# Performance work log

Hardware: AMD Instinct MI355X
Metric: run time of the kernel (lower is better)

## Reference

```python
import jax, jax.numpy as jnp
import numpy as np

B, T, D = 4, 2048, 1024
H, DH = 16, 64

def setup_inputs() -> dict:
    key = jax.random.key(0)
    k1, k2, k3 = jax.random.split(key, 3)
    x = jax.random.normal(k1, (B, T, D), dtype=jnp.float32)
    # nn.Linear weights stored [out, in]; we keep that convention
    w_attn = jax.random.normal(k2, (3 * D, D), dtype=jnp.float32) * (1.0 / np.sqrt(D))
    w_proj = jax.random.normal(k3, (D, D), dtype=jnp.float32) * (1.0 / np.sqrt(D))
    return {"x": x, "w_attn": w_attn, "w_proj": w_proj}

def reference(x, w_attn, w_proj):
    Bx, Tx, Dx = x.shape
    qkv = jnp.einsum('btd,ed->bte', x, w_attn)            # [B,T,3D]
    qkv = qkv.reshape(Bx, Tx, 3, H, DH)
    q = qkv[:, :, 0].transpose(0, 2, 1, 3)                # [B,H,T,DH]
    k = qkv[:, :, 1].transpose(0, 2, 1, 3)
    v = qkv[:, :, 2].transpose(0, 2, 1, 3)
    scale = 1.0 / np.sqrt(DH).astype(np.float32)
    att = jnp.einsum('bhqd,bhkd->bhqk', q, k) * scale     # [B,H,T,T]
    causal = jnp.tril(jnp.ones((Tx, Tx), dtype=bool))
    att = jnp.where(causal[None, None], att, jnp.float32(-jnp.inf))
    att = jax.nn.softmax(att, axis=-1)
    y = jnp.einsum('bhqk,bhkd->bhqd', att, v)             # [B,H,T,DH]
    y = y.transpose(0, 2, 1, 3).reshape(Bx, Tx, Dx)       # [B,T,D]
    y = jnp.einsum('btd,ed->bte', y, w_proj)
    return y
```

## Files before the change

kernel.cpp:

```cpp
#include <hip/hip_runtime.h>

typedef unsigned short u16;
typedef __bf16 bf16x8 __attribute__((ext_vector_type(8)));
typedef float floatx4 __attribute__((ext_vector_type(4)));

__device__ inline u16 f2bf(float x) {
    unsigned int u = __builtin_bit_cast(unsigned int, x);
    return (u16)((u + 0x7FFFu + ((u >> 16) & 1u)) >> 16);
}

__device__ inline floatx4 fzero() {
    floatx4 z = {0.f, 0.f, 0.f, 0.f};
    return z;
}

#if defined(__has_builtin)
#if __has_builtin(__builtin_amdgcn_exp2f)
#define EXP2F(x) __builtin_amdgcn_exp2f(x)
#endif
#endif
#ifndef EXP2F
#define EXP2F(x) exp2f(x)
#endif

template <bool F32>
__device__ inline bf16x8 ld8(const void* base, size_t off) {
    if constexpr (F32) {
        const float* p = (const float*)base + off;
        float4 a = *(const float4*)p;
        float4 b = *(const float4*)(p + 4);
        union { u16 u[8]; bf16x8 v; } t;
        t.u[0] = f2bf(a.x); t.u[1] = f2bf(a.y); t.u[2] = f2bf(a.z); t.u[3] = f2bf(a.w);
        t.u[4] = f2bf(b.x); t.u[5] = f2bf(b.y); t.u[6] = f2bf(b.z); t.u[7] = f2bf(b.w);
        return t.v;
    } else {
        return *(const bf16x8*)((const u16*)base + off);
    }
}

__global__ __launch_bounds__(256) void cvt_f32_bf16(const float* __restrict__ src,
                                                    u16* __restrict__ dst, int n8) {
    int i = blockIdx.x * 256 + threadIdx.x;
    if (i >= n8) return;
    dst += (size_t)i * 8;
    *(bf16x8*)dst = ld8<true>(src, (size_t)i * 8);
}

#define BK 32

template <bool AF32, bool BF32, bool CF32>
__global__ __launch_bounds__(256) void gemm_bt(const void* __restrict__ Ap,
                                               const void* __restrict__ Bp,
                                               void* __restrict__ Cp,
                                               int M, int N, int K) {
    __shared__ alignas(16) u16 As[128 * BK];
    __shared__ alignas(16) u16 Bs[128 * BK];

    const int tid  = threadIdx.x;
    const int lane = tid & 63;
    const int wave = tid >> 6;
    const int wm = (wave >> 1) * 64;
    const int wn = (wave & 1) * 64;
    const int tm = blockIdx.y * 128;
    const int tn = blockIdx.x * 128;
    const int l15 = lane & 15;
    const int l4  = lane >> 4;

    const int srow = tid >> 2;
    const int scol = (tid & 3) * 8;

    floatx4 acc[4][4];
#pragma unroll
    for (int i = 0; i < 4; i++)
#pragma unroll
        for (int j = 0; j < 4; j++) acc[i][j] = fzero();

    for (int k0 = 0; k0 < K; k0 += BK) {
        bf16x8 av[2], bv[2];
#pragma unroll
        for (int q = 0; q < 2; q++) {
            av[q] = ld8<AF32>(Ap, (size_t)(tm + srow + q * 64) * K + k0 + scol);
            bv[q] = ld8<BF32>(Bp, (size_t)(tn + srow + q * 64) * K + k0 + scol);
        }
        __syncthreads();
#pragma unroll
        for (int q = 0; q < 2; q++) {
            *(bf16x8*)&As[(srow + q * 64) * BK + scol] = av[q];
            *(bf16x8*)&Bs[(srow + q * 64) * BK + scol] = bv[q];
        }
        __syncthreads();

        bf16x8 af[4], bf[4];
#pragma unroll
        for (int i = 0; i < 4; i++)
            af[i] = *(const bf16x8*)&As[(wm + i * 16 + l15) * BK + l4 * 8];
#pragma unroll
        for (int j = 0; j < 4; j++)
            bf[j] = *(const bf16x8*)&Bs[(wn + j * 16 + l15) * BK + l4 * 8];
#pragma unroll
        for (int i = 0; i < 4; i++)
#pragma unroll
            for (int j = 0; j < 4; j++)
                acc[i][j] = __builtin_amdgcn_mfma_f32_16x16x32_bf16(af[i], bf[j], acc[i][j], 0, 0, 0);
    }

#pragma unroll
    for (int i = 0; i < 4; i++)
#pragma unroll
        for (int j = 0; j < 4; j++)
#pragma unroll
            for (int r = 0; r < 4; r++) {
                int row = tm + wm + i * 16 + l4 * 4 + r;
                int col = tn + wn + j * 16 + l15;
                if constexpr (CF32)
                    ((float*)Cp)[(size_t)row * N + col] = acc[i][j][r];
                else
                    ((u16*)Cp)[(size_t)row * N + col] = f2bf(acc[i][j][r]);
            }
}

__global__ __launch_bounds__(256) void transpose_v(const u16* __restrict__ qkv,
                                                   u16* __restrict__ vT) {
    __shared__ alignas(16) u16 Ts[64 * 80];
    const int bh = blockIdx.x;
    const int b = bh >> 4, h = bh & 15;
    const int t0 = blockIdx.y * 64;
    const int tid = threadIdx.x;
    const int r = tid >> 3;
    const int c = tid & 7;
#pragma unroll
    for (int p = 0; p < 2; p++) {
        int tr = r + p * 32;
        *(bf16x8*)&Ts[tr * 80 + c * 8] =
            *(const bf16x8*)&qkv[(size_t)(b * 2048 + t0 + tr) * 3072 + 2048 + h * 64 + c * 8];
    }
    __syncthreads();
#pragma unroll
    for (int p = 0; p < 2; p++) {
        int dr = r + p * 32;
        union { u16 u[8]; bf16x8 v; } t;
#pragma unroll
        for (int i = 0; i < 8; i++) t.u[i] = Ts[(c * 8 + i) * 80 + dr];
        *(bf16x8*)&vT[(size_t)bh * 131072 + (size_t)dr * 2048 + t0 + c * 8] = t.v;
    }
}

#define AST 88

template <bool USE_VT>
__global__ __launch_bounds__(256) void attn2(const u16* __restrict__ qkv,
                                             const u16* __restrict__ vT,
                                             u16* __restrict__ y) {
    const int T = 2048, CW = 3072;
    __shared__ alignas(16) u16 KP[64 * AST];
    __shared__ alignas(16) u16 Vt[64 * AST];

    const int tid  = threadIdx.x;
    const int lane = tid & 63;
    const int wave = tid >> 6;
    const int l15 = lane & 15;
    const int l4  = lane >> 4;

    const int bh = blockIdx.x;
    const int qt = 31 - blockIdx.y;
    const int b = bh >> 4, h = bh & 15;
    const int q0 = qt * 64;

    const size_t base = (size_t)b * T * CW + h * 64;
    const u16* qp = qkv + base;
    const u16* kp = qkv + base + 1024;
    const u16* vp = qkv + base + 2048;
    const u16* vtp = USE_VT ? (vT + (size_t)bh * 131072) : nullptr;

    bf16x8 qf[2];
    {
        int qrow = q0 + wave * 16 + l15;
        qf[0] = *(const bf16x8*)&qp[(size_t)qrow * CW + l4 * 8];
        qf[1] = *(const bf16x8*)&qp[(size_t)qrow * CW + 32 + l4 * 8];
    }

    const float C2 = 0.18033688f;
    float lrow[4] = {0.f, 0.f, 0.f, 0.f};
    floatx4 Oacc[4];
#pragma unroll
    for (int cf = 0; cf < 4; cf++) Oacc[cf] = fzero();

    const int sr = tid >> 3;
    const int sc = tid & 7;

    for (int kt = 0; kt <= qt; kt++) {
        const int t0 = kt * 64;
        __syncthreads();

#pragma unroll
        for (int p = 0; p < 2; p++) {
            int tr = sr + p * 32;
            *(bf16x8*)&KP[tr * AST + sc * 8] =
                *(const bf16x8*)&kp[(size_t)(t0 + tr) * CW + sc * 8];
        }
        if constexpr (USE_VT) {
#pragma unroll
            for (int p = 0; p < 2; p++) {
                int dr = sr + p * 32;
                *(bf16x8*)&Vt[dr * AST + sc * 8] =
                    *(const bf16x8*)&vtp[(size_t)dr * 2048 + t0 + sc * 8];
            }
        } else {
            int dh = tid & 63;
            int tb = (tid >> 6) * 8;
#pragma unroll
            for (int p = 0; p < 2; p++) {
                int tl = tb + p * 32;
                union { u16 u[8]; bf16x8 v; } tmp;
#pragma unroll
                for (int i = 0; i < 8; i++)
                    tmp.u[i] = vp[(size_t)(t0 + tl + i) * CW + dh];
                *(bf16x8*)&Vt[dh * AST + tl] = tmp.v;
            }
        }
        __syncthreads();

        floatx4 sfr[4];
#pragma unroll
        for (int j = 0; j < 4; j++) {
            bf16x8 k0f = *(const bf16x8*)&KP[(j * 16 + l15) * AST + l4 * 8];
            bf16x8 k1f = *(const bf16x8*)&KP[(j * 16 + l15) * AST + 32 + l4 * 8];
            floatx4 s = fzero();
            s = __builtin_amdgcn_mfma_f32_16x16x32_bf16(qf[0], k0f, s, 0, 0, 0);
            s = __builtin_amdgcn_mfma_f32_16x16x32_bf16(qf[1], k1f, s, 0, 0, 0);
            sfr[j] = s;
        }
        bf16x8 v0f[4], v1f[4];
#pragma unroll
        for (int cf = 0; cf < 4; cf++) {
            v0f[cf] = *(const bf16x8*)&Vt[(cf * 16 + l15) * AST + l4 * 8];
            v1f[cf] = *(const bf16x8*)&Vt[(cf * 16 + l15) * AST + 32 + l4 * 8];
        }

        float pj[4][4];
        if (kt == qt) {
#pragma unroll
            for (int j = 0; j < 4; j++)
#pragma unroll
                for (int r = 0; r < 4; r++) {
                    int qrow = q0 + wave * 16 + l4 * 4 + r;
                    int krow = t0 + j * 16 + l15;
                    float e = (krow <= qrow) ? sfr[j][r] * C2 : -1.0e30f;
                    pj[j][r] = EXP2F(e);
                }
        } else {
#pragma unroll
            for (int j = 0; j < 4; j++)
#pragma unroll
                for (int r = 0; r < 4; r++)
                    pj[j][r] = EXP2F(sfr[j][r] * C2);
        }
#pragma unroll
        for (int r = 0; r < 4; r++)
            lrow[r] += (pj[0][r] + pj[1][r]) + (pj[2][r] + pj[3][r]);

        __syncthreads();
#pragma unroll
        for (int j = 0; j < 4; j++)
#pragma unroll
            for (int r = 0; r < 4; r++)
                KP[(wave * 16 + l4 * 4 + r) * AST + j * 16 + l15] = f2bf(pj[j][r]);
        __syncthreads();

        bf16x8 pf0 = *(const bf16x8*)&KP[(wave * 16 + l15) * AST + l4 * 8];
        bf16x8 pf1 = *(const bf16x8*)&KP[(wave * 16 + l15) * AST + 32 + l4 * 8];
#pragma unroll
        for (int cf = 0; cf < 4; cf++) {
            Oacc[cf] = __builtin_amdgcn_mfma_f32_16x16x32_bf16(pf0, v0f[cf], Oacc[cf], 0, 0, 0);
            Oacc[cf] = __builtin_amdgcn_mfma_f32_16x16x32_bf16(pf1, v1f[cf], Oacc[cf], 0, 0, 0);
        }
    }

#pragma unroll
    for (int r = 0; r < 4; r++) {
#pragma unroll
        for (int off = 1; off < 16; off <<= 1)
            lrow[r] += __shfl_xor(lrow[r], off, 64);
    }
#pragma unroll
    for (int r = 0; r < 4; r++) {
        float inv = 1.0f / lrow[r];
        int qrow = q0 + wave * 16 + l4 * 4 + r;
        size_t orow = ((size_t)b * T + qrow) * 1024 + h * 64;
#pragma unroll
        for (int cf = 0; cf < 4; cf++)
            y[orow + cf * 16 + l15] = f2bf(Oacc[cf][r] * inv);
    }
}

extern "C" void kernel_launch(void* const* d_in, const int* in_sizes, int n_in,
                              void* d_out, int out_size, void* d_ws, size_t ws_size,
                              hipStream_t stream) {
    const float* x      = (const float*)d_in[0];
    const float* w_attn = (const float*)d_in[1];
    const float* w_proj = (const float*)d_in[2];
    float* out = (float*)d_out;

    const size_t QKV = (size_t)8192 * 3072;
    const size_t Y   = (size_t)8192 * 1024;
    const size_t VTE = (size_t)64 * 64 * 2048;
    const size_t XB  = (size_t)8192 * 1024;
    const size_t WAB = (size_t)3072 * 1024;
    const size_t WPB = (size_t)1024 * 1024;

    u16* qkv = (u16*)d_ws;
    u16* yb  = qkv + QKV;

    const bool full = ws_size >= (QKV + Y + VTE + XB + WAB + WPB) * sizeof(u16);
    const bool mid  = ws_size >= (QKV + Y + VTE) * sizeof(u16);
    if (ws_size < (QKV + Y) * sizeof(u16)) return;

    dim3 blk(256);
    dim3 g1(3072 / 128, 8192 / 128), g2(1024 / 128, 8192 / 128);
    dim3 ga(64, 32);

    if (full) {
        u16* vT  = yb + Y;
        u16* xb  = vT + VTE;
        u16* wab = xb + XB;
        u16* wpb = wab + WAB;
        cvt_f32_bf16<<<(XB / 8 + 255) / 256, blk, 0, stream>>>(x, xb, (int)(XB / 8));
        cvt_f32_bf16<<<(WAB / 8 + 255) / 256, blk, 0, stream>>>(w_attn, wab, (int)(WAB / 8));
        cvt_f32_bf16<<<(WPB / 8 + 255) / 256, blk, 0, stream>>>(w_proj, wpb, (int)(WPB / 8));
        gemm_bt<false, false, false><<<g1, blk, 0, stream>>>(xb, wab, qkv, 8192, 3072, 1024);
        transpose_v<<<ga, blk, 0, stream>>>(qkv, vT);
        attn2<true><<<ga, blk, 0, stream>>>(qkv, vT, yb);
        gemm_bt<false, false, true><<<g2, blk, 0, stream>>>(yb, wpb, out, 8192, 1024, 1024);
    } else if (mid) {
        u16* vT = yb + Y;
        gemm_bt<true, true, false><<<g1, blk, 0, stream>>>(x, w_attn, qkv, 8192, 3072, 1024);
        transpose_v<<<ga, blk, 0, stream>>>(qkv, vT);
        attn2<true><<<ga, blk, 0, stream>>>(qkv, vT, yb);
        gemm_bt<false, true, true><<<g2, blk, 0, stream>>>(yb, w_proj, out, 8192, 1024, 1024);
    } else {
        gemm_bt<true, true, false><<<g1, blk, 0, stream>>>(x, w_attn, qkv, 8192, 3072, 1024);
        attn2<false><<<ga, blk, 0, stream>>>(qkv, nullptr, yb);
        gemm_bt<false, true, true><<<g2, blk, 0, stream>>>(yb, w_proj, out, 8192, 1024, 1024);
    }
}
```

Baseline: 285.3 us.

## Restructure attention to 128-row query tiles with per-wave P buffers

The attention kernel now handles 128 query rows per block (32 per wave, in two 16-row groups), so each staged K/V tile is reused by twice as many queries. The P tile goes through a per-wave shared buffer, which removes two block-wide barriers per key tile. The kernel computes S transposed (K times Q) and pre-scales Q by the softmax constant, and skips the MFMAs for row groups that lie fully above the causal diagonal. It also writes the output as vectorised bf16x4 stores. In exchange it uses more registers and shared memory (launch bounds 256,4), and the grid has half as many blocks, with more per-block imbalance along the causal diagonal.

```diff
diff --git a/kernel.cpp b/kernel.cpp
--- a/kernel.cpp
+++ b/kernel.cpp
@@ -2,7 +2,9 @@
 
 typedef unsigned short u16;
 typedef __bf16 bf16x8 __attribute__((ext_vector_type(8)));
+typedef __bf16 bf16x4 __attribute__((ext_vector_type(4)));
 typedef float floatx4 __attribute__((ext_vector_type(4)));
+typedef float floatx8 __attribute__((ext_vector_type(8)));
 
 __device__ inline u16 f2bf(float x) {
     unsigned int u = __builtin_bit_cast(unsigned int, x);
@@ -22,6 +24,12 @@
 #ifndef EXP2F
 #define EXP2F(x) exp2f(x)
 #endif
+
+__device__ inline bf16x8 scale8(bf16x8 v, float s) {
+    floatx8 f = __builtin_convertvector(v, floatx8);
+    f *= s;
+    return __builtin_convertvector(f, bf16x8);
+}
 
 template <bool F32>
 __device__ inline bf16x8 ld8(const void* base, size_t off) {
@@ -145,15 +153,17 @@
     }
 }
 
-#define AST 88
+#define AST 72
+#define PST 72
 
 template <bool USE_VT>
-__global__ __launch_bounds__(256) void attn2(const u16* __restrict__ qkv,
-                                             const u16* __restrict__ vT,
-                                             u16* __restrict__ y) {
+__global__ __launch_bounds__(256, 4) void attn3(const u16* __restrict__ qkv,
+                                                const u16* __restrict__ vT,
+                                                u16* __restrict__ y) {
     const int T = 2048, CW = 3072;
-    __shared__ alignas(16) u16 KP[64 * AST];
+    __shared__ alignas(16) u16 Kt[64 * AST];
     __shared__ alignas(16) u16 Vt[64 * AST];
+    __shared__ alignas(16) u16 Pw[4][32 * PST];
 
     const int tid  = threadIdx.x;
     const int lane = tid & 63;
@@ -162,40 +172,44 @@
     const int l4  = lane >> 4;
 
     const int bh = blockIdx.x;
-    const int qt = 31 - blockIdx.y;
+    const int qi = 15 - blockIdx.y;
     const int b = bh >> 4, h = bh & 15;
-    const int q0 = qt * 64;
+    const int q0 = qi * 128;
 
     const size_t base = (size_t)b * T * CW + h * 64;
     const u16* qp = qkv + base;
     const u16* kp = qkv + base + 1024;
     const u16* vp = qkv + base + 2048;
-    const u16* vtp = USE_VT ? (vT + (size_t)bh * 131072) : nullptr;
-
-    bf16x8 qf[2];
-    {
-        int qrow = q0 + wave * 16 + l15;
-        qf[0] = *(const bf16x8*)&qp[(size_t)qrow * CW + l4 * 8];
-        qf[1] = *(const bf16x8*)&qp[(size_t)qrow * CW + 32 + l4 * 8];
-    }
+    const u16* vtp = vT + (size_t)bh * ((size_t)64 * 2048);
 
     const float C2 = 0.18033688f;
-    float lrow[4] = {0.f, 0.f, 0.f, 0.f};
-    floatx4 Oacc[4];
-#pragma unroll
-    for (int cf = 0; cf < 4; cf++) Oacc[cf] = fzero();
-
-    const int sr = tid >> 3;
-    const int sc = tid & 7;
-
-    for (int kt = 0; kt <= qt; kt++) {
+    bf16x8 qf[2][2];
+#pragma unroll
+    for (int g = 0; g < 2; g++) {
+        int qrow = q0 + wave * 32 + g * 16 + l15;
+#pragma unroll
+        for (int hh = 0; hh < 2; hh++)
+            qf[g][hh] = scale8(*(const bf16x8*)&qp[(size_t)qrow * CW + hh * 32 + l4 * 8], C2);
+    }
+
+    float lsum[2] = {0.f, 0.f};
+    floatx4 acc[2][4];
+#pragma unroll
+    for (int g = 0; g < 2; g++)
+#pragma unroll
+        for (int mf = 0; mf < 4; mf++) acc[g][mf] = fzero();
+
+    const int sr = tid >> 3, sc = tid & 7;
+    const int nkt = 2 * qi + 2;
+
+    for (int kt = 0; kt < nkt; kt++) {
         const int t0 = kt * 64;
         __syncthreads();
 
 #pragma unroll
         for (int p = 0; p < 2; p++) {
             int tr = sr + p * 32;
-            *(bf16x8*)&KP[tr * AST + sc * 8] =
+            *(bf16x8*)&Kt[tr * AST + sc * 8] =
                 *(const bf16x8*)&kp[(size_t)(t0 + tr) * CW + sc * 8];
         }
         if constexpr (USE_VT) {
@@ -220,76 +234,82 @@
         }
         __syncthreads();
 
-        floatx4 sfr[4];
-#pragma unroll
-        for (int j = 0; j < 4; j++) {
-            bf16x8 k0f = *(const bf16x8*)&KP[(j * 16 + l15) * AST + l4 * 8];
-            bf16x8 k1f = *(const bf16x8*)&KP[(j * 16 + l15) * AST + 32 + l4 * 8];
-            floatx4 s = fzero();
-            s = __builtin_amdgcn_mfma_f32_16x16x32_bf16(qf[0], k0f, s, 0, 0, 0);
-            s = __builtin_amdgcn_mfma_f32_16x16x32_bf16(qf[1], k1f, s, 0, 0, 0);
-            sfr[j] = s;
-        }
-        bf16x8 v0f[4], v1f[4];
-#pragma unroll
-        for (int cf = 0; cf < 4; cf++) {
-            v0f[cf] = *(const bf16x8*)&Vt[(cf * 16 + l15) * AST + l4 * 8];
-            v1f[cf] = *(const bf16x8*)&Vt[(cf * 16 + l15) * AST + 32 + l4 * 8];
-        }
-
-        float pj[4][4];
-        if (kt == qt) {
-#pragma unroll
-            for (int j = 0; j < 4; j++)
+        bf16x8 kf[4][2];
+#pragma unroll
+        for (int mf = 0; mf < 4; mf++)
+#pragma unroll
+            for (int hh = 0; hh < 2; hh++)
+                kf[mf][hh] = *(const bf16x8*)&Kt[(mf * 16 + l15) * AST + hh * 32 + l4 * 8];
+
+        bool act[2];
+#pragma unroll
+        for (int g = 0; g < 2; g++) {
+            const int qlo = wave * 32 + g * 16;
+            act[g] = (t0 <= q0 + qlo + 15);
+            if (!act[g]) continue;
+
+            floatx4 s[4];
+#pragma unroll
+            for (int mf = 0; mf < 4; mf++) {
+                floatx4 t = fzero();
+                t = __builtin_amdgcn_mfma_f32_16x16x32_bf16(kf[mf][0], qf[g][0], t, 0, 0, 0);
+                t = __builtin_amdgcn_mfma_f32_16x16x32_bf16(kf[mf][1], qf[g][1], t, 0, 0, 0);
+                s[mf] = t;
+            }
+
+            const bool domask = (t0 + 63 > q0 + qlo);
+            const int qrow = q0 + qlo + l15;
+            float part = 0.f;
+#pragma unroll
+            for (int mf = 0; mf < 4; mf++) {
+                floatx4 pv;
 #pragma unroll
                 for (int r = 0; r < 4; r++) {
-                    int qrow = q0 + wave * 16 + l4 * 4 + r;
-                    int krow = t0 + j * 16 + l15;
-                    float e = (krow <= qrow) ? sfr[j][r] * C2 : -1.0e30f;
-                    pj[j][r] = EXP2F(e);
+                    int key = t0 + mf * 16 + l4 * 4 + r;
+                    float e = EXP2F(s[mf][r]);
+                    pv[r] = (domask && key > qrow) ? 0.f : e;
                 }
-        } else {
-#pragma unroll
-            for (int j = 0; j < 4; j++)
-#pragma unroll
-                for (int r = 0; r < 4; r++)
-                    pj[j][r] = EXP2F(sfr[j][r] * C2);
-        }
-#pragma unroll
-        for (int r = 0; r < 4; r++)
-            lrow[r] += (pj[0][r] + pj[1][r]) + (pj[2][r] + pj[3][r]);
-
-        __syncthreads();
-#pragma unroll
-        for (int j = 0; j < 4; j++)
-#pragma unroll
-            for (int r = 0; r < 4; r++)
-                KP[(wave * 16 + l4 * 4 + r) * AST + j * 16 + l15] = f2bf(pj[j][r]);
-        __syncthreads();
-
-        bf16x8 pf0 = *(const bf16x8*)&KP[(wave * 16 + l15) * AST + l4 * 8];
-        bf16x8 pf1 = *(const bf16x8*)&KP[(wave * 16 + l15) * AST + 32 + l4 * 8];
-#pragma unroll
-        for (int cf = 0; cf < 4; cf++) {
-            Oacc[cf] = __builtin_amdgcn_mfma_f32_16x16x32_bf16(pf0, v0f[cf], Oacc[cf], 0, 0, 0);
-            Oacc[cf] = __builtin_amdgcn_mfma_f32_16x16x32_bf16(pf1, v1f[cf], Oacc[cf], 0, 0, 0);
-        }
-    }
-
-#pragma unroll
-    for (int r = 0; r < 4; r++) {
-#pragma unroll
-        for (int off = 1; off < 16; off <<= 1)
-            lrow[r] += __shfl_xor(lrow[r], off, 64);
-    }
-#pragma unroll
-    for (int r = 0; r < 4; r++) {
-        float inv = 1.0f / lrow[r];
-        int qrow = q0 + wave * 16 + l4 * 4 + r;
+                part += (pv[0] + pv[1]) + (pv[2] + pv[3]);
+                *(bf16x4*)&Pw[wave][(g * 16 + l15) * PST + mf * 16 + l4 * 4] =
+                    __builtin_convertvector(pv, bf16x4);
+            }
+            lsum[g] += part;
+        }
+
+        bf16x8 pf[2][2];
+#pragma unroll
+        for (int g = 0; g < 2; g++)
+            if (act[g]) {
+#pragma unroll
+                for (int hh = 0; hh < 2; hh++)
+                    pf[g][hh] = *(const bf16x8*)&Pw[wave][(g * 16 + l15) * PST + hh * 32 + l4 * 8];
+            }
+
+#pragma unroll
+        for (int mf = 0; mf < 4; mf++) {
+            bf16x8 v0 = *(const bf16x8*)&Vt[(mf * 16 + l15) * AST + l4 * 8];
+            bf16x8 v1 = *(const bf16x8*)&Vt[(mf * 16 + l15) * AST + 32 + l4 * 8];
+#pragma unroll
+            for (int g = 0; g < 2; g++)
+                if (act[g]) {
+                    acc[g][mf] = __builtin_amdgcn_mfma_f32_16x16x32_bf16(v0, pf[g][0], acc[g][mf], 0, 0, 0);
+                    acc[g][mf] = __builtin_amdgcn_mfma_f32_16x16x32_bf16(v1, pf[g][1], acc[g][mf], 0, 0, 0);
+                }
+        }
+    }
+
+#pragma unroll
+    for (int g = 0; g < 2; g++) {
+        lsum[g] += __shfl_xor(lsum[g], 16, 64);
+        lsum[g] += __shfl_xor(lsum[g], 32, 64);
+        float inv = 1.0f / lsum[g];
+        int qrow = q0 + wave * 32 + g * 16 + l15;
         size_t orow = ((size_t)b * T + qrow) * 1024 + h * 64;
 #pragma unroll
-        for (int cf = 0; cf < 4; cf++)
-            y[orow + cf * 16 + l15] = f2bf(Oacc[cf][r] * inv);
+        for (int mf = 0; mf < 4; mf++) {
+            floatx4 o = acc[g][mf] * inv;
+            *(bf16x4*)&y[orow + mf * 16 + l4 * 4] = __builtin_convertvector(o, bf16x4);
+        }
     }
 }
 
@@ -317,7 +337,7 @@
 
     dim3 blk(256);
     dim3 g1(3072 / 128, 8192 / 128), g2(1024 / 128, 8192 / 128);
-    dim3 ga(64, 32);
+    dim3 gt(64, 32), ga(64, 16);
 
     if (full) {
         u16* vT  = yb + Y;
@@ -328,18 +348,18 @@
         cvt_f32_bf16<<<(WAB / 8 + 255) / 256, blk, 0, stream>>>(w_attn, wab, (int)(WAB / 8));
         cvt_f32_bf16<<<(WPB / 8 + 255) / 256, blk, 0, stream>>>(w_proj, wpb, (int)(WPB / 8));
         gemm_bt<false, false, false><<<g1, blk, 0, stream>>>(xb, wab, qkv, 8192, 3072, 1024);
-        transpose_v<<<ga, blk, 0, stream>>>(qkv, vT);
-        attn2<true><<<ga, blk, 0, stream>>>(qkv, vT, yb);
+        transpose_v<<<gt, blk, 0, stream>>>(qkv, vT);
+        attn3<true><<<ga, blk, 0, stream>>>(qkv, vT, yb);
         gemm_bt<false, false, true><<<g2, blk, 0, stream>>>(yb, wpb, out, 8192, 1024, 1024);
     } else if (mid) {
         u16* vT = yb + Y;
         gemm_bt<true, true, false><<<g1, blk, 0, stream>>>(x, w_attn, qkv, 8192, 3072, 1024);
-        transpose_v<<<ga, blk, 0, stream>>>(qkv, vT);
-        attn2<true><<<ga, blk, 0, stream>>>(qkv, vT, yb);
+        transpose_v<<<gt, blk, 0, stream>>>(qkv, vT);
+        attn3<true><<<ga, blk, 0, stream>>>(qkv, vT, yb);
         gemm_bt<false, true, true><<<g2, blk, 0, stream>>>(yb, w_proj, out, 8192, 1024, 1024);
     } else {
         gemm_bt<true, true, false><<<g1, blk, 0, stream>>>(x, w_attn, qkv, 8192, 3072, 1024);
-        attn2<false><<<ga, blk, 0, stream>>>(qkv, nullptr, yb);
+        attn3<false><<<ga, blk, 0, stream>>>(qkv, nullptr, yb);
         gemm_bt<false, true, true><<<g2, blk, 0, stream>>>(yb, w_proj, out, 8192, 1024, 1024);
     }
 }
```

Result: slower. 355.4 us (+24.6%).
